# Optimization experiments

Hardware: AMD Instinct MI355X
Metric: run time of the kernel (lower is better)

## Reference

```python
import jax, jax.numpy as jnp
import numpy as np

IGNORE = 255


def setup_inputs() -> dict:
    key = jax.random.key(0)
    k1, k2 = jax.random.split(key)
    B, C, H, W = 4, 19, 512, 512
    out = jax.random.normal(k1, (B, C, H, W), dtype=jnp.float32)
    gt = jax.random.randint(k2, (B, H, W), 0, C, dtype=jnp.int64)
    return {"out": out, "gt": gt}


def _lovasz_softmax_flat(probas, labels):
    # probas: [P, C] softmax probabilities, labels: [P] int
    P, C = probas.shape
    valid = labels != IGNORE  # [P]
    # per-class foreground indicator (masked by valid)
    fg = ((labels[:, None] == jnp.arange(C)[None, :]) & valid[:, None]).astype(probas.dtype)  # [P, C]
    errors = jnp.abs(fg - probas)  # [P, C], values in [0, 1]
    # push ignored pixels to the end of the descending sort (error < 0)
    errors = jnp.where(valid[:, None], errors, -1.0)
    order = jnp.argsort(-errors, axis=0)  # [P, C] descending perm per class
    errors_sorted = jnp.take_along_axis(errors, order, axis=0)
    fg_sorted = jnp.take_along_axis(fg, order, axis=0)
    valid_sorted = jnp.take_along_axis(jnp.broadcast_to(valid[:, None], (P, C)), order, axis=0)
    # zero out ignored pixels' (suffix) contribution
    errors_sorted = jnp.where(valid_sorted, errors_sorted, 0.0)
    # lovasz_grad per class (ignored suffix has fg=0 and errors=0, so it is inert)
    gts = jnp.sum(fg_sorted, axis=0)  # [C]
    csum_fg = jnp.cumsum(fg_sorted, axis=0)
    intersection = gts[None, :] - csum_fg
    union = gts[None, :] + jnp.cumsum(1.0 - fg_sorted, axis=0)
    jaccard = 1.0 - intersection / union
    grad = jnp.concatenate([jaccard[:1], jnp.diff(jaccard, axis=0)], axis=0)  # [P, C]
    loss_c = jnp.sum(errors_sorted * grad, axis=0)  # [C]
    # classes='present': average over classes that appear among valid pixels
    present = gts > 0
    n_present = jnp.maximum(jnp.sum(present.astype(probas.dtype)), 1.0)
    return jnp.sum(jnp.where(present, loss_c, 0.0)) / n_present


def reference(out, gt):
    B, C, H, W = out.shape
    probas = jax.nn.softmax(out, axis=1)  # [B, C, H, W]
    probas_flat = jnp.transpose(probas, (0, 2, 3, 1)).reshape(-1, C)  # [P, C]
    labels_flat = gt.reshape(-1)  # [P]
    return _lovasz_softmax_flat(probas_flat, labels_flat)
```

## Files before the change

kernel.cpp:

```cpp
#include <hip/hip_runtime.h>
#include <stdint.h>


#define IGNORE_LBL 255
typedef unsigned long long u64;
constexpr int C_CLS = 19;
constexpr int NB = 128;
constexpr int NBT = C_CLS * NB;
constexpr int NBT_PAIR = NBT / 2;
constexpr int PART_STRIDE = NBT + NBT_PAIR;
constexpr int HW_C = 512 * 512;
constexpr int HIST_GRID = 1024;
constexpr int HIST_NT = 512;
constexpr int RED_Q = 8;
constexpr float ESCALE = 1023.f;

__device__ __forceinline__ int err_bin(float e) {
    unsigned u = __float_as_uint(e);
    if (u >= 0x3F800000u) return NB - 1;
    if (u < 0x3C800000u) return 0;
    int m = (int)(u >> 23) - 120;
    return (1 << m) - 1 + (int)((u & 0x7FFFFFu) >> (23 - m));
}

__global__ __launch_bounds__(HIST_NT, 6)
void lovasz_hist_kernel(const float* __restrict__ logits,
                        const int* __restrict__ gt,
                        unsigned* __restrict__ part) {
    __shared__ unsigned h_ec[2 * NBT];
    __shared__ unsigned h_fg[NBT];
    __shared__ unsigned h_b0[C_CLS * 8];
    for (int i = threadIdx.x; i < 2 * NBT; i += HIST_NT) h_ec[i] = 0u;
    for (int i = threadIdx.x; i < NBT; i += HIST_NT) h_fg[i] = 0u;
    if (threadIdx.x < C_CLS * 8) h_b0[threadIdx.x] = 0u;
    __syncthreads();

    const int gid = blockIdx.x * HIST_NT + threadIdx.x;
    const int p0 = gid * 2;
    const int2 lbl2 = *(const int2*)(gt + p0);
    const int b = p0 >> 18;
    const int hw = p0 & (HW_C - 1);
    const float2* base =
        (const float2*)(logits + (size_t)b * C_CLS * HW_C + hw);
    const int cp = (threadIdx.x >> 5) & 1;
    const int b0s = threadIdx.x & 7;

    float2 v[C_CLS];
    float mx0 = -3.4e38f, mx1 = -3.4e38f;
#pragma unroll
    for (int c = 0; c < C_CLS; ++c) {
        v[c] = base[(size_t)c * (HW_C / 2)];
        mx0 = fmaxf(mx0, v[c].x);
        mx1 = fmaxf(mx1, v[c].y);
    }
    float s0 = 0.f, s1 = 0.f;
#pragma unroll
    for (int c = 0; c < C_CLS; ++c) {
        v[c].x = __expf(v[c].x - mx0);
        v[c].y = __expf(v[c].y - mx1);
        s0 += v[c].x;
        s1 += v[c].y;
    }
    const float inv0 = 1.0f / s0;
    const float inv1 = 1.0f / s1;

    const bool val0 = (lbl2.x != IGNORE_LBL);
    const bool val1 = (lbl2.y != IGNORE_LBL);
    int fgbin0 = 0, fgbin1 = 0;

#pragma unroll
    for (int c = 0; c < C_CLS; ++c) {
        if (val0) {
            float prob = v[c].x * inv0;
            bool fg = (c == lbl2.x);
            float e = fmaxf(fg ? (1.0f - prob) : prob, 0.0f);
            unsigned eq = __float2uint_rn(e * ESCALE);
            int bin = err_bin(e);
            if (fg) fgbin0 = c * NB + bin;
            unsigned* addr = (bin == 0) ? &h_b0[c * 8 + b0s]
                                        : &h_ec[(c * NB + bin) * 2 + cp];
            atomicAdd(addr, (1u << 21) | eq);
        }
        if (val1) {
            float prob = v[c].y * inv1;
            bool fg = (c == lbl2.y);
            float e = fmaxf(fg ? (1.0f - prob) : prob, 0.0f);
            unsigned eq = __float2uint_rn(e * ESCALE);
            int bin = err_bin(e);
            if (fg) fgbin1 = c * NB + bin;
            unsigned* addr = (bin == 0) ? &h_b0[c * 8 + b0s]
                                        : &h_ec[(c * NB + bin) * 2 + cp];
            atomicAdd(addr, (1u << 21) | eq);
        }
    }
    if (val0) atomicAdd(&h_fg[fgbin0], 1u);
    if (val1) atomicAdd(&h_fg[fgbin1], 1u);
    __syncthreads();

    unsigned* outp = part + (size_t)blockIdx.x * PART_STRIDE;
    for (int i = threadIdx.x; i < NBT; i += HIST_NT) {
        unsigned m = h_ec[2 * i] + h_ec[2 * i + 1];
        if ((i & (NB - 1)) == 0) {
            const int c = i / NB;
#pragma unroll
            for (int j = 0; j < 8; ++j) m += h_b0[c * 8 + j];
        }
        outp[i] = m;
    }
    for (int i = threadIdx.x; i < NBT_PAIR; i += HIST_NT)
        outp[NBT + i] = h_fg[2 * i] | (h_fg[2 * i + 1] << 16);
}

__global__ __launch_bounds__(NB)
void lovasz_reduce_kernel(const unsigned* __restrict__ part,
                          unsigned* __restrict__ red_es,
                          u64* __restrict__ red_cf,
                          unsigned* __restrict__ acc) {
    if (blockIdx.x == 0 && threadIdx.x < 4) acc[threadIdx.x] = 0u;
    const int q = blockIdx.x / C_CLS;
    const int seg = blockIdx.x % C_CLS;
    const int bin = seg * NB + threadIdx.x;
    const int fgw = NBT + (bin >> 1);
    const int fgsh = (bin & 1) * 16;
    const int p0 = q * (HIST_GRID / RED_Q);
    unsigned es = 0, cn = 0, fgc = 0;
#pragma unroll 4
    for (int p = p0; p < p0 + HIST_GRID / RED_Q; ++p) {
        unsigned x = part[(size_t)p * PART_STRIDE + bin];
        es += x & 0x1FFFFFu;
        cn += x >> 21;
        fgc += (part[(size_t)p * PART_STRIDE + fgw] >> fgsh) & 0xFFFFu;
    }
    red_es[(size_t)q * NBT + bin] = es;
    red_cf[(size_t)q * NBT + bin] = (u64)cn | ((u64)fgc << 32);
}

__global__ __launch_bounds__(NB)
void lovasz_scan_kernel(const unsigned* __restrict__ red_es,
                        const u64* __restrict__ red_cf,
                        float* __restrict__ loss_acc,
                        int* __restrict__ pres_acc,
                        unsigned* __restrict__ done_ctr,
                        float* __restrict__ out) {
    const int c = blockIdx.x;
    const int t = threadIdx.x;
    const int lane = t & 63;
    const int wave = t >> 6;

    __shared__ u64 wtot[2];
    __shared__ u64 sh_total;

    const int db = NB - 1 - t;
    const size_t bo = (size_t)c * NB + db;
    u64 es = 0, nf = 0;
#pragma unroll
    for (int q = 0; q < RED_Q; ++q) {
        es += (u64)red_es[(size_t)q * NBT + bo];
        nf += red_cf[(size_t)q * NBT + bo];
    }
    const double mys = (double)es * (1.0 / (double)ESCALE);

    u64 incl = nf;
#pragma unroll
    for (int o = 1; o < 64; o <<= 1) {
        u64 u = __shfl_up(incl, o, 64);
        if (lane >= o) incl += u;
    }
    if (lane == 63) wtot[wave] = incl;
    __syncthreads();
    if (t == 0) {
        u64 w0 = wtot[0];
        wtot[0] = 0; sh_total = w0 + wtot[1];
        wtot[1] = w0;
    }
    __syncthreads();

    const long long G = (long long)(sh_total >> 32);
    const u64 excl = wtot[wave] + (incl - nf);

    double lsum = 0.0;
    {
        long long n_b = (long long)(nf & 0xffffffffull);
        if (n_b > 0 && G > 0) {
            long long f_b = (long long)(nf >> 32);
            long long k0 = (long long)(excl & 0xffffffffull);
            long long F0 = (long long)(excl >> 32);
            long long I0 = G - F0;
            long long U0 = G + k0 - F0;
            long long F1 = F0 + f_b;
            long long I1 = G - F1;
            long long U1 = G + (k0 + n_b) - F1;
            double dJ = (double)(I0 * U1 - I1 * U0) / ((double)U0 * (double)U1);
            lsum = (mys / (double)n_b) * dJ;
        }
    }

    __shared__ double dred[2];
#pragma unroll
    for (int o = 32; o > 0; o >>= 1) lsum += __shfl_down(lsum, o, 64);
    if (lane == 0) dred[wave] = lsum;
    __syncthreads();
    if (t == 0) {
        double tot = dred[0] + dred[1];
        if (G > 0) {
            atomicAdd(loss_acc, (float)tot);
            atomicAdd(pres_acc, 1);
        }
        __threadfence();
        unsigned d = atomicAdd(done_ctr, 1u);
        if (d == C_CLS - 1) {
            float lv = atomicAdd(loss_acc, 0.0f);
            int pv = atomicAdd(pres_acc, 0);
            out[0] = lv / fmaxf((float)pv, 1.0f);
        }
    }
}

extern "C" void kernel_launch(void* const* d_in, const int* in_sizes, int n_in,
                              void* d_out, int out_size, void* d_ws, size_t ws_size,
                              hipStream_t stream) {
    const float* logits = (const float*)d_in[0];
    const int* gt = (const int*)d_in[1];
    float* out = (float*)d_out;

    size_t partBytes = (size_t)HIST_GRID * PART_STRIDE * sizeof(unsigned);
    size_t partPad = (partBytes + 255) & ~(size_t)255;
    size_t redEsBytes = (size_t)RED_Q * NBT * sizeof(unsigned);
    size_t redEsPad = (redEsBytes + 255) & ~(size_t)255;
    size_t redCfBytes = (size_t)RED_Q * NBT * sizeof(u64);
    size_t redCfPad = (redCfBytes + 255) & ~(size_t)255;
    unsigned* part = (unsigned*)d_ws;
    unsigned* red_es = (unsigned*)((char*)d_ws + partPad);
    u64* red_cf = (u64*)((char*)d_ws + partPad + redEsPad);
    unsigned* acc = (unsigned*)((char*)d_ws + partPad + redEsPad + redCfPad);
    float* loss_acc = (float*)&acc[0];
    int* pres_acc = (int*)&acc[1];
    unsigned* done_ctr = &acc[2];

    lovasz_hist_kernel<<<HIST_GRID, HIST_NT, 0, stream>>>(logits, gt, part);
    lovasz_reduce_kernel<<<RED_Q * C_CLS, NB, 0, stream>>>(part, red_es, red_cf, acc);
    lovasz_scan_kernel<<<C_CLS, NB, 0, stream>>>(red_es, red_cf,
                                                 loss_acc, pres_acc, done_ctr, out);
}
```

Baseline: 135.8 us.

## Loop histogram blocks over four sweeps and drop the intermediate reduce kernel

The histogram kernel now launches 256 blocks that each process four pixel-pair sweeps, so there are four times fewer per-block partial histograms. Since there are fewer partials, the separate reduce kernel is removed and the scan kernel sums all 256 partials directly. The per-block record is repacked to hold the error sum plus count and fg count in 16-bit fields. The error quantization scale is halved so the larger per-block counts fit the packed fields, which gives up some precision in the error sums. The scan kernel now does a serial 256-iteration read over partials on only 19 blocks, and fewer hist blocks may lower latency hiding on the 256-CU part.

Measured after the change: 193.6 us. 1.42x slower.

```diff
diff --git a/kernel.cpp b/kernel.cpp
--- a/kernel.cpp
+++ b/kernel.cpp
@@ -7,13 +7,12 @@
 constexpr int C_CLS = 19;
 constexpr int NB = 128;
 constexpr int NBT = C_CLS * NB;
-constexpr int NBT_PAIR = NBT / 2;
-constexpr int PART_STRIDE = NBT + NBT_PAIR;
+constexpr int PART_STRIDE = 2 * NBT;
 constexpr int HW_C = 512 * 512;
-constexpr int HIST_GRID = 1024;
+constexpr int HIST_GRID = 256;
 constexpr int HIST_NT = 512;
-constexpr int RED_Q = 8;
-constexpr float ESCALE = 1023.f;
+constexpr int SWEEPS = 4;
+constexpr float ESCALE = 511.f;
 
 __device__ __forceinline__ int err_bin(float e) {
     unsigned u = __float_as_uint(e);
@@ -26,118 +25,103 @@
 __global__ __launch_bounds__(HIST_NT, 6)
 void lovasz_hist_kernel(const float* __restrict__ logits,
                         const int* __restrict__ gt,
-                        unsigned* __restrict__ part) {
+                        unsigned* __restrict__ part,
+                        unsigned* __restrict__ acc) {
     __shared__ unsigned h_ec[2 * NBT];
     __shared__ unsigned h_fg[NBT];
     __shared__ unsigned h_b0[C_CLS * 8];
     for (int i = threadIdx.x; i < 2 * NBT; i += HIST_NT) h_ec[i] = 0u;
     for (int i = threadIdx.x; i < NBT; i += HIST_NT) h_fg[i] = 0u;
     if (threadIdx.x < C_CLS * 8) h_b0[threadIdx.x] = 0u;
+    if (blockIdx.x == 0 && threadIdx.x < 4) acc[threadIdx.x] = 0u;
     __syncthreads();
 
     const int gid = blockIdx.x * HIST_NT + threadIdx.x;
-    const int p0 = gid * 2;
-    const int2 lbl2 = *(const int2*)(gt + p0);
-    const int b = p0 >> 18;
-    const int hw = p0 & (HW_C - 1);
-    const float2* base =
-        (const float2*)(logits + (size_t)b * C_CLS * HW_C + hw);
     const int cp = (threadIdx.x >> 5) & 1;
     const int b0s = threadIdx.x & 7;
 
-    float2 v[C_CLS];
-    float mx0 = -3.4e38f, mx1 = -3.4e38f;
-#pragma unroll
-    for (int c = 0; c < C_CLS; ++c) {
-        v[c] = base[(size_t)c * (HW_C / 2)];
-        mx0 = fmaxf(mx0, v[c].x);
-        mx1 = fmaxf(mx1, v[c].y);
-    }
-    float s0 = 0.f, s1 = 0.f;
-#pragma unroll
-    for (int c = 0; c < C_CLS; ++c) {
-        v[c].x = __expf(v[c].x - mx0);
-        v[c].y = __expf(v[c].y - mx1);
-        s0 += v[c].x;
-        s1 += v[c].y;
-    }
-    const float inv0 = 1.0f / s0;
-    const float inv1 = 1.0f / s1;
-
-    const bool val0 = (lbl2.x != IGNORE_LBL);
-    const bool val1 = (lbl2.y != IGNORE_LBL);
-    int fgbin0 = 0, fgbin1 = 0;
-
-#pragma unroll
-    for (int c = 0; c < C_CLS; ++c) {
-        if (val0) {
-            float prob = v[c].x * inv0;
-            bool fg = (c == lbl2.x);
-            float e = fmaxf(fg ? (1.0f - prob) : prob, 0.0f);
-            unsigned eq = __float2uint_rn(e * ESCALE);
-            int bin = err_bin(e);
-            if (fg) fgbin0 = c * NB + bin;
-            unsigned* addr = (bin == 0) ? &h_b0[c * 8 + b0s]
-                                        : &h_ec[(c * NB + bin) * 2 + cp];
-            atomicAdd(addr, (1u << 21) | eq);
-        }
-        if (val1) {
-            float prob = v[c].y * inv1;
-            bool fg = (c == lbl2.y);
-            float e = fmaxf(fg ? (1.0f - prob) : prob, 0.0f);
-            unsigned eq = __float2uint_rn(e * ESCALE);
-            int bin = err_bin(e);
-            if (fg) fgbin1 = c * NB + bin;
-            unsigned* addr = (bin == 0) ? &h_b0[c * 8 + b0s]
-                                        : &h_ec[(c * NB + bin) * 2 + cp];
-            atomicAdd(addr, (1u << 21) | eq);
-        }
-    }
-    if (val0) atomicAdd(&h_fg[fgbin0], 1u);
-    if (val1) atomicAdd(&h_fg[fgbin1], 1u);
+    for (int sweep = 0; sweep < SWEEPS; ++sweep) {
+        const int p0 = (sweep * (HIST_GRID * HIST_NT) + gid) * 2;
+        const int2 lbl2 = *(const int2*)(gt + p0);
+        const int b = p0 >> 18;
+        const int hw = p0 & (HW_C - 1);
+        const float2* base =
+            (const float2*)(logits + (size_t)b * C_CLS * HW_C + hw);
+
+        float2 v[C_CLS];
+        float mx0 = -3.4e38f, mx1 = -3.4e38f;
+#pragma unroll
+        for (int c = 0; c < C_CLS; ++c) {
+            v[c] = base[(size_t)c * (HW_C / 2)];
+            mx0 = fmaxf(mx0, v[c].x);
+            mx1 = fmaxf(mx1, v[c].y);
+        }
+        float s0 = 0.f, s1 = 0.f;
+#pragma unroll
+        for (int c = 0; c < C_CLS; ++c) {
+            v[c].x = __expf(v[c].x - mx0);
+            v[c].y = __expf(v[c].y - mx1);
+            s0 += v[c].x;
+            s1 += v[c].y;
+        }
+        const float inv0 = 1.0f / s0;
+        const float inv1 = 1.0f / s1;
+
+        const bool val0 = (lbl2.x != IGNORE_LBL);
+        const bool val1 = (lbl2.y != IGNORE_LBL);
+        int fgbin0 = 0, fgbin1 = 0;
+
+#pragma unroll
+        for (int c = 0; c < C_CLS; ++c) {
+            if (val0) {
+                float prob = v[c].x * inv0;
+                bool fg = (c == lbl2.x);
+                float e = fmaxf(fg ? (1.0f - prob) : prob, 0.0f);
+                unsigned eq = __float2uint_rn(e * ESCALE);
+                int bin = err_bin(e);
+                if (fg) fgbin0 = c * NB + bin;
+                unsigned* addr = (bin == 0) ? &h_b0[c * 8 + b0s]
+                                            : &h_ec[(c * NB + bin) * 2 + cp];
+                atomicAdd(addr, (1u << 20) | eq);
+            }
+            if (val1) {
+                float prob = v[c].y * inv1;
+                bool fg = (c == lbl2.y);
+                float e = fmaxf(fg ? (1.0f - prob) : prob, 0.0f);
+                unsigned eq = __float2uint_rn(e * ESCALE);
+                int bin = err_bin(e);
+                if (fg) fgbin1 = c * NB + bin;
+                unsigned* addr = (bin == 0) ? &h_b0[c * 8 + b0s]
+                                            : &h_ec[(c * NB + bin) * 2 + cp];
+                atomicAdd(addr, (1u << 20) | eq);
+            }
+        }
+        if (val0) atomicAdd(&h_fg[fgbin0], 1u);
+        if (val1) atomicAdd(&h_fg[fgbin1], 1u);
+    }
     __syncthreads();
 
     unsigned* outp = part + (size_t)blockIdx.x * PART_STRIDE;
     for (int i = threadIdx.x; i < NBT; i += HIST_NT) {
-        unsigned m = h_ec[2 * i] + h_ec[2 * i + 1];
+        unsigned e0 = h_ec[2 * i], e1 = h_ec[2 * i + 1];
+        unsigned es = (e0 & 0xFFFFFu) + (e1 & 0xFFFFFu);
+        unsigned cn = (e0 >> 20) + (e1 >> 20);
         if ((i & (NB - 1)) == 0) {
             const int c = i / NB;
 #pragma unroll
-            for (int j = 0; j < 8; ++j) m += h_b0[c * 8 + j];
-        }
-        outp[i] = m;
-    }
-    for (int i = threadIdx.x; i < NBT_PAIR; i += HIST_NT)
-        outp[NBT + i] = h_fg[2 * i] | (h_fg[2 * i + 1] << 16);
+            for (int j = 0; j < 8; ++j) {
+                unsigned x = h_b0[c * 8 + j];
+                es += x & 0xFFFFFu;
+                cn += x >> 20;
+            }
+        }
+        outp[i] = es;
+        outp[NBT + i] = cn | (h_fg[i] << 16);
+    }
 }
 
 __global__ __launch_bounds__(NB)
-void lovasz_reduce_kernel(const unsigned* __restrict__ part,
-                          unsigned* __restrict__ red_es,
-                          u64* __restrict__ red_cf,
-                          unsigned* __restrict__ acc) {
-    if (blockIdx.x == 0 && threadIdx.x < 4) acc[threadIdx.x] = 0u;
-    const int q = blockIdx.x / C_CLS;
-    const int seg = blockIdx.x % C_CLS;
-    const int bin = seg * NB + threadIdx.x;
-    const int fgw = NBT + (bin >> 1);
-    const int fgsh = (bin & 1) * 16;
-    const int p0 = q * (HIST_GRID / RED_Q);
-    unsigned es = 0, cn = 0, fgc = 0;
-#pragma unroll 4
-    for (int p = p0; p < p0 + HIST_GRID / RED_Q; ++p) {
-        unsigned x = part[(size_t)p * PART_STRIDE + bin];
-        es += x & 0x1FFFFFu;
-        cn += x >> 21;
-        fgc += (part[(size_t)p * PART_STRIDE + fgw] >> fgsh) & 0xFFFFu;
-    }
-    red_es[(size_t)q * NBT + bin] = es;
-    red_cf[(size_t)q * NBT + bin] = (u64)cn | ((u64)fgc << 32);
-}
-
-__global__ __launch_bounds__(NB)
-void lovasz_scan_kernel(const unsigned* __restrict__ red_es,
-                        const u64* __restrict__ red_cf,
+void lovasz_scan_kernel(const unsigned* __restrict__ part,
                         float* __restrict__ loss_acc,
                         int* __restrict__ pres_acc,
                         unsigned* __restrict__ done_ctr,
@@ -151,13 +135,18 @@
     __shared__ u64 sh_total;
 
     const int db = NB - 1 - t;
-    const size_t bo = (size_t)c * NB + db;
-    u64 es = 0, nf = 0;
-#pragma unroll
-    for (int q = 0; q < RED_Q; ++q) {
-        es += (u64)red_es[(size_t)q * NBT + bo];
-        nf += red_cf[(size_t)q * NBT + bo];
-    }
+    const int bo = c * NB + db;
+    u64 es = 0;
+    unsigned cn = 0, fgc = 0;
+#pragma unroll 8
+    for (int p = 0; p < HIST_GRID; ++p) {
+        const unsigned* bp = part + (size_t)p * PART_STRIDE;
+        es += bp[bo];
+        unsigned w = bp[NBT + bo];
+        cn += w & 0xFFFFu;
+        fgc += w >> 16;
+    }
+    u64 nf = (u64)cn | ((u64)fgc << 32);
     const double mys = (double)es * (1.0 / (double)ESCALE);
 
     u64 incl = nf;
@@ -225,20 +214,13 @@
 
     size_t partBytes = (size_t)HIST_GRID * PART_STRIDE * sizeof(unsigned);
     size_t partPad = (partBytes + 255) & ~(size_t)255;
-    size_t redEsBytes = (size_t)RED_Q * NBT * sizeof(unsigned);
-    size_t redEsPad = (redEsBytes + 255) & ~(size_t)255;
-    size_t redCfBytes = (size_t)RED_Q * NBT * sizeof(u64);
-    size_t redCfPad = (redCfBytes + 255) & ~(size_t)255;
     unsigned* part = (unsigned*)d_ws;
-    unsigned* red_es = (unsigned*)((char*)d_ws + partPad);
-    u64* red_cf = (u64*)((char*)d_ws + partPad + redEsPad);
-    unsigned* acc = (unsigned*)((char*)d_ws + partPad + redEsPad + redCfPad);
+    unsigned* acc = (unsigned*)((char*)d_ws + partPad);
     float* loss_acc = (float*)&acc[0];
     int* pres_acc = (int*)&acc[1];
     unsigned* done_ctr = &acc[2];
 
-    lovasz_hist_kernel<<<HIST_GRID, HIST_NT, 0, stream>>>(logits, gt, part);
-    lovasz_reduce_kernel<<<RED_Q * C_CLS, NB, 0, stream>>>(part, red_es, red_cf, acc);
-    lovasz_scan_kernel<<<C_CLS, NB, 0, stream>>>(red_es, red_cf,
-                                                 loss_acc, pres_acc, done_ctr, out);
-}
+    lovasz_hist_kernel<<<HIST_GRID, HIST_NT, 0, stream>>>(logits, gt, part, acc);
+    lovasz_scan_kernel<<<C_CLS, NB, 0, stream>>>(part, loss_acc, pres_acc,
+                                                 done_ctr, out);
+}
```
